# Kernel tuning notes

Hardware: AMD Instinct MI355X
Metric: run time of the kernel (lower is better)

## Reference

```python
import jax, jax.numpy as jnp
import numpy as np

NEG_SLOPE = 0.01  # torch F.leaky_relu default


def setup_inputs() -> dict:
    key = jax.random.key(0)
    k1, k2, k3, k4 = jax.random.split(key, 4)
    N, E, R, D = 100000, 1250000, 16, 64
    ego_embed = jax.random.normal(k1, (N, D), dtype=jnp.float32) * 0.1
    relation_weights = jax.random.normal(k2, (R, D, D), dtype=jnp.float32) * (1.0 / np.sqrt(D))
    edge_index = jax.random.randint(k3, (2, E), 0, N, dtype=jnp.int32)
    edge_type = jax.random.randint(k4, (E,), 0, R, dtype=jnp.int32)
    return {"ego_embed": ego_embed, "relation_weights": relation_weights,
            "edge_index": edge_index, "edge_type": edge_type}


def reference(ego_embed, relation_weights, edge_index, edge_type):
    head, tail = edge_index[0], edge_index[1]
    n_entities = ego_embed.shape[0]
    # Transform every node by every relation once ([R,N,D]) instead of
    # materializing the per-edge [E,D,D] weight gather the torch bmm implies;
    # same math: transformed_head[e] = ego_embed[head[e]] @ W[edge_type[e]].
    transformed_all = jnp.einsum('nd,rdk->rnk', ego_embed, relation_weights)
    transformed_head = transformed_all[edge_type, head]        # [E, D]
    tail_emb = ego_embed[tail]                                  # [E, D]
    scores = jax.nn.leaky_relu(jnp.sum(transformed_head * tail_emb, axis=1),
                               negative_slope=NEG_SLOPE)        # [E]
    exp_scores = jnp.exp(scores)                                # unnormalized attention
    denom = jax.ops.segment_sum(exp_scores, head, num_segments=n_entities)[head]
    norm_att = exp_scores / denom                               # segment softmax
    weighted = tail_emb * norm_att[:, None]                     # [E, D]
    # scatter_mean: segment sum / per-segment edge count (clamped to 1)
    summed = jax.ops.segment_sum(weighted, head, num_segments=n_entities)
    counts = jax.ops.segment_sum(jnp.ones_like(exp_scores), head, num_segments=n_entities)
    return summed / jnp.maximum(counts, 1.0)[:, None]
```

## Files before the change

kernel.cpp:

```cpp
#include <hip/hip_runtime.h>
#include <stdint.h>

#define NEG_SLOPE 0.01f
#define HPG 32
#define TSTR 72
#define BSH 8
#define NBMAX 512
#define K1CH 8192
#define CAP2 8192

typedef float f32x4 __attribute__((ext_vector_type(4)));
typedef short short8 __attribute__((ext_vector_type(8)));
typedef unsigned int u32;

#define DPPADD(v, ctrl) ((v) + __int_as_float(__builtin_amdgcn_update_dpp( \
        0, __float_as_int(v), (ctrl), 0xF, 0xF, true)))

__device__ inline short f2bf(float f) {
    union { float f; uint32_t u; } x; x.f = f;
    uint32_t r = x.u + 0x7FFF + ((x.u >> 16) & 1);
    return (short)(r >> 16);
}
__device__ inline float bf2f(unsigned short u) {
    union { uint32_t u; float f; } x; x.u = ((uint32_t)u) << 16; return x.f;
}

__global__ void __launch_bounds__(512) kA(
        const int* __restrict__ head, const int* __restrict__ tail,
        const int* __restrict__ etype, int E, int NB, int nblk,
        u32* __restrict__ staging, int* bucket_cur,
        const float* __restrict__ ego, unsigned short* __restrict__ ego_bf,
        int NE8, const float* __restrict__ rw, short* __restrict__ wfrag,
        int* __restrict__ head_off, int N) {
    int t = threadIdx.x;
    int bid = blockIdx.x;
    if (bid < nblk) {
        __shared__ int lcnt[NBMAX], lbase[NBMAX], lfill[NBMAX];
        for (int b = t; b < NBMAX; b += 512) lcnt[b] = 0;
        __syncthreads();
        long long base = (long long)bid * K1CH;
        #pragma unroll
        for (int s = 0; s < K1CH / 512; ++s) {
            long long e = base + t + s * 512;
            if (e < E) atomicAdd(&lcnt[head[e] >> BSH], 1);
        }
        __syncthreads();
        for (int b = t; b < NB; b += 512) {
            int c = lcnt[b];
            lbase[b] = c ? atomicAdd(&bucket_cur[b], c) : 0;
            lfill[b] = 0;
        }
        __syncthreads();
        #pragma unroll
        for (int s = 0; s < K1CH / 512; ++s) {
            long long e = base + t + s * 512;
            if (e < E) {
                int h = head[e];
                int bk = h >> BSH;
                int rk = atomicAdd(&lfill[bk], 1);
                int pos = lbase[bk] + rk;
                if (pos >= CAP2) pos = CAP2 - 1;
                staging[(size_t)bk * CAP2 + pos] =
                    (u32)tail[e] | ((u32)etype[e] << 20) | ((u32)(h & 255) << 24);
            }
        }
    } else {
        int ib = bid - nblk;
        if (ib == 0 && t == 0) head_off[N] = E;
        if (ib < 16) {
            int r = ib;
            int lane = t & 63;
            int c = lane & 15, q = lane >> 4;
            int pair = t >> 6;
            int t4 = pair >> 1, kh = pair & 1;
            int m = t4 * 16 + c;
            short8 f;
            for (int j = 0; j < 8; ++j) {
                int k = kh * 32 + q * 8 + j;
                f[j] = f2bf(rw[r * 4096 + k * 64 + m]);
            }
            *(short8*)(wfrag + ((size_t)((r * 4 + t4) * 2 + kh) * 64 + lane) * 8) = f;
        }
        int i = ib * 512 + t;
        if (i < NE8) {
            const float4* p = (const float4*)ego + (size_t)i * 2;
            float4 a = p[0], b = p[1];
            short8 v;
            v[0] = f2bf(a.x); v[1] = f2bf(a.y); v[2] = f2bf(a.z); v[3] = f2bf(a.w);
            v[4] = f2bf(b.x); v[5] = f2bf(b.y); v[6] = f2bf(b.z); v[7] = f2bf(b.w);
            *(short8*)(ego_bf + (size_t)i * 8) = v;
        }
    }
}

__global__ void __launch_bounds__(512) kB(
        const u32* __restrict__ staging, const int* __restrict__ bucket_cur,
        int* __restrict__ head_off, int* __restrict__ recs2, int N, int NB) {
    __shared__ int pre[NBMAX];
    __shared__ int lcnt[256], lofs[256], lfill[256];
    __shared__ u32 lrec[CAP2];
    int t = threadIdx.x;
    int b = blockIdx.x;
    if (t < 256) lcnt[t] = 0;
    int v = (t < NB) ? bucket_cur[t] : 0;
    pre[t] = v;
    __syncthreads();
    for (int off = 1; off < 512; off <<= 1) {
        int x = (t >= off) ? pre[t - off] : 0;
        __syncthreads();
        pre[t] += x;
        __syncthreads();
    }
    int cnt_raw = bucket_cur[b];
    int base_g = pre[b] - cnt_raw;
    int cntb = cnt_raw > CAP2 ? CAP2 : cnt_raw;
    int hbase = b << BSH;
    const u32* sb = staging + (size_t)b * CAP2;
    for (int t0 = t; t0 < cntb; t0 += 512) {
        u32 rec = sb[t0];
        lrec[t0] = rec;
        atomicAdd(&lcnt[rec >> 24], 1);
    }
    __syncthreads();
    if (t < 64) {
        int cl[4]; int cs = 0;
        #pragma unroll
        for (int j = 0; j < 4; ++j) { cl[j] = lcnt[t * 4 + j]; cs += cl[j]; }
        int inc = cs;
        for (int off = 1; off < 64; off <<= 1) {
            int u = __shfl_up(inc, off);
            if (t >= off) inc += u;
        }
        int run = inc - cs;
        #pragma unroll
        for (int j = 0; j < 4; ++j) {
            lofs[t * 4 + j] = run; lfill[t * 4 + j] = run; run += cl[j];
        }
    }
    __syncthreads();
    if (t < 256 && hbase + t < N)
        head_off[hbase + t] = base_g + lofs[t];
    for (int t0 = t; t0 < cntb; t0 += 512) {
        u32 rec = lrec[t0];
        int rk = atomicAdd(&lfill[rec >> 24], 1);
        recs2[base_g + rk] = (int)(rec & 0xFFFFFF);
    }
}

__global__ void __launch_bounds__(512, 4) k4_fused(
        const unsigned short* __restrict__ ego_bf,
        const short* __restrict__ wfrag,
        const int* __restrict__ recs2,
        const int* __restrict__ head_off,
        float* __restrict__ out, int N) {
    __shared__ unsigned short T[16 * HPG * TSTR];
    int tid = threadIdx.x;
    int wave = tid >> 6;
    int lane = tid & 63;
    int c = lane & 15, q = lane >> 4;
    int hb = blockIdx.x * HPG;

    for (int t = 0; t < 2; ++t) {
        int r = wave * 2 + t;
        const short* wp = wfrag + (size_t)r * 4096;
        short8 wf[4][2];
        #pragma unroll
        for (int t4 = 0; t4 < 4; ++t4)
            #pragma unroll
            for (int kh = 0; kh < 2; ++kh)
                wf[t4][kh] = *(const short8*)(wp + ((size_t)((t4 * 2 + kh) * 64 + lane)) * 8);
        #pragma unroll
        for (int hf = 0; hf < 2; ++hf) {
            int hrow = hb + hf * 16 + c;
            if (hrow >= N) hrow = N - 1;
            const unsigned short* hr = ego_bf + (size_t)hrow * 64;
            short8 b0 = *(const short8*)(hr + q * 8);
            short8 b1 = *(const short8*)(hr + 32 + q * 8);
            #pragma unroll
            for (int t4 = 0; t4 < 4; ++t4) {
                f32x4 a = {0.f, 0.f, 0.f, 0.f};
                a = __builtin_amdgcn_mfma_f32_16x16x32_bf16(wf[t4][0], b0, a, 0, 0, 0);
                a = __builtin_amdgcn_mfma_f32_16x16x32_bf16(wf[t4][1], b1, a, 0, 0, 0);
                ushort4 us;
                us.x = (unsigned short)f2bf(a[0]);
                us.y = (unsigned short)f2bf(a[1]);
                us.z = (unsigned short)f2bf(a[2]);
                us.w = (unsigned short)f2bf(a[3]);
                *(ushort4*)&T[(size_t)(r * HPG + hf * 16 + c) * TSTR + t4 * 16 + q * 4] = us;
            }
        }
    }
    __syncthreads();

    int hql = wave * 4 + q;
    int h = hb + hql;
    if (h >= N) return;
    int lq = c;
    int g2 = lq >> 3, c8 = lq & 7;
    int qb = q * 16;
    int s0 = head_off[h], s1 = head_off[h + 1];
    int cnt = s1 - s0;
    int nbt = (cnt + 15) >> 4;
    float acc[8] = {0.f, 0.f, 0.f, 0.f, 0.f, 0.f, 0.f, 0.f};
    float den = 0.f;

    auto loadRec = [&](int b) -> int {
        if (b >= nbt) return 0;
        int idx = s0 + b * 16 + lq;
        return (idx < s1) ? recs2[idx] : 0;
    };

    int rjA[8]; short8 rowsA[8];
    int recL1;
    {
        int recL0 = loadRec(0);
        #pragma unroll
        for (int j = 0; j < 8; ++j) rjA[j] = __shfl(recL0, qb + j * 2 + g2);
        #pragma unroll
        for (int j = 0; j < 8; ++j)
            rowsA[j] = *(const short8*)(ego_bf + (size_t)(rjA[j] & 0xFFFFF) * 64 + c8 * 8);
        recL1 = loadRec(1);
    }
    for (int b = 0; b < nbt; ++b) {
        int recL2 = loadRec(b + 2);
        int rjB[8]; short8 rowsB[8];
        #pragma unroll
        for (int j = 0; j < 8; ++j) rjB[j] = __shfl(recL1, qb + j * 2 + g2);
        #pragma unroll
        for (int j = 0; j < 8; ++j)
            rowsB[j] = *(const short8*)(ego_bf + (size_t)(rjB[j] & 0xFFFFF) * 64 + c8 * 8);
        int ng = s1 - (s0 + b * 16); if (ng > 16) ng = 16;
        #pragma unroll
        for (int sIt = 0; sIt < 8; ++sIt) {
            if (sIt * 2 < ng) {
                short8 trw = *(const short8*)&T[(size_t)(((u32)rjA[sIt] >> 20) * HPG + hql) * TSTR + c8 * 8];
                float rf[8];
                float sa = 0.f, sb = 0.f;
                #pragma unroll
                for (int k = 0; k < 4; ++k) {
                    rf[k] = bf2f((unsigned short)rowsA[sIt][k]);
                    sa += rf[k] * bf2f((unsigned short)trw[k]);
                }
                #pragma unroll
                for (int k = 4; k < 8; ++k) {
                    rf[k] = bf2f((unsigned short)rowsA[sIt][k]);
                    sb += rf[k] * bf2f((unsigned short)trw[k]);
                }
                float s = sa + sb;
                s = DPPADD(s, 0xB1);
                s = DPPADD(s, 0x4E);
                s = DPPADD(s, 0x141);
                float lr = s > 0.f ? s : NEG_SLOPE * s;
                float w = (sIt * 2 + g2 < ng) ? __expf(lr) : 0.f;
                den += w;
                #pragma unroll
                for (int k = 0; k < 8; ++k) acc[k] += w * rf[k];
            }
        }
        recL1 = recL2;
        #pragma unroll
        for (int j = 0; j < 8; ++j) { rjA[j] = rjB[j]; rowsA[j] = rowsB[j]; }
    }
    den = DPPADD(den, 0x128);
    #pragma unroll
    for (int k = 0; k < 8; ++k) acc[k] = DPPADD(acc[k], 0x128);
    if (g2 == 0) {
        float sc = (cnt > 0) ? 1.f / (den * (float)cnt) : 0.f;
        float4 v0 = {acc[0] * sc, acc[1] * sc, acc[2] * sc, acc[3] * sc};
        float4 v1 = {acc[4] * sc, acc[5] * sc, acc[6] * sc, acc[7] * sc};
        float* op = out + (size_t)h * 64 + c8 * 8;
        *(float4*)op = v0;
        *(float4*)(op + 4) = v1;
    }
}

extern "C" void kernel_launch(void* const* d_in, const int* in_sizes, int n_in,
                              void* d_out, int out_size, void* d_ws, size_t ws_size,
                              hipStream_t stream) {
    const float* ego = (const float*)d_in[0];
    const float* rw  = (const float*)d_in[1];
    const int* eidx  = (const int*)d_in[2];
    const int* etyp  = (const int*)d_in[3];
    int N = in_sizes[0] / 64;
    int E = in_sizes[3];
    const int* head = eidx;
    const int* tail = eidx + E;
    float* out = (float*)d_out;

    char* ws = (char*)d_ws;
    size_t o = 0;
    auto take = [&](size_t bytes) -> char* {
        char* p = ws + o;
        o = (o + bytes + 255) & ~(size_t)255;
        return p;
    };
    int NB = (N + (1 << BSH) - 1) >> BSH;
    if (NB > NBMAX) NB = NBMAX;
    int nblk = (E + K1CH - 1) / K1CH;
    int NE8 = N * 8;
    int nbI = (NE8 + 511) / 512;
    if (nbI < 16) nbI = 16;
    unsigned short* ego_bf = (unsigned short*)take((size_t)N * 64 * 2);
    short* wfrag    = (short*)take(16 * 4096 * 2);
    int* recs2      = (int*)take((size_t)E * 4);
    u32* staging    = (u32*)take((size_t)NB * CAP2 * 4);
    int* bucket_cur = (int*)take(NBMAX * 4);
    int* head_off   = (int*)take((size_t)(N + 1) * 4);
    (void)ws_size; (void)n_in; (void)out_size;

    hipMemsetAsync(bucket_cur, 0, NBMAX * 4, stream);
    kA<<<nblk + nbI, 512, 0, stream>>>(head, tail, etyp, E, NB, nblk,
                                       staging, bucket_cur,
                                       ego, ego_bf, NE8, rw, wfrag,
                                       head_off, N);
    kB<<<NB, 512, 0, stream>>>(staging, bucket_cur, head_off, recs2, N, NB);
    k4_fused<<<(N + HPG - 1) / HPG, 512, 0, stream>>>(ego_bf, wfrag, recs2,
                                                      head_off, out, N);
}
```

Baseline: 186.8 us.

## Fuse per-bucket sort into main kernel using 32-head buckets matching block tile

Shrinks the head buckets to 32 heads so each bucket lines up exactly with one k4_fused block. The second counting-sort kernel (kB) and the global recs2/head_off arrays go away. Each block now loads its bucket's staging records into LDS, builds per-head offsets with an LDS histogram and wave scan, and reads edge records from LDS instead of global memory. This removes a kernel launch and a full write and read of the edge array. The cost is 3200 buckets with 12KB+ LDS counters in kA, a per-bucket capacity cap of 1024 that would overflow on skewed heads, and more LDS use in the main kernel.

```diff
diff --git a/kernel.cpp b/kernel.cpp
--- a/kernel.cpp
+++ b/kernel.cpp
@@ -4,10 +4,10 @@
 #define NEG_SLOPE 0.01f
 #define HPG 32
 #define TSTR 72
-#define BSH 8
-#define NBMAX 512
-#define K1CH 8192
-#define CAP2 8192
+#define BSH 5
+#define NBMX 3200
+#define K1CH 16384
+#define CAP3 1024
 
 typedef float f32x4 __attribute__((ext_vector_type(4)));
 typedef short short8 __attribute__((ext_vector_type(8)));
@@ -30,13 +30,12 @@
         const int* __restrict__ etype, int E, int NB, int nblk,
         u32* __restrict__ staging, int* bucket_cur,
         const float* __restrict__ ego, unsigned short* __restrict__ ego_bf,
-        int NE8, const float* __restrict__ rw, short* __restrict__ wfrag,
-        int* __restrict__ head_off, int N) {
+        int NE8, const float* __restrict__ rw, short* __restrict__ wfrag) {
     int t = threadIdx.x;
     int bid = blockIdx.x;
     if (bid < nblk) {
-        __shared__ int lcnt[NBMAX], lbase[NBMAX], lfill[NBMAX];
-        for (int b = t; b < NBMAX; b += 512) lcnt[b] = 0;
+        __shared__ int lcnt[NBMX], lbase[NBMX], lfill[NBMX];
+        for (int b = t; b < NBMX; b += 512) lcnt[b] = 0;
         __syncthreads();
         long long base = (long long)bid * K1CH;
         #pragma unroll
@@ -59,14 +58,13 @@
                 int bk = h >> BSH;
                 int rk = atomicAdd(&lfill[bk], 1);
                 int pos = lbase[bk] + rk;
-                if (pos >= CAP2) pos = CAP2 - 1;
-                staging[(size_t)bk * CAP2 + pos] =
-                    (u32)tail[e] | ((u32)etype[e] << 20) | ((u32)(h & 255) << 24);
+                if (pos >= CAP3) pos = CAP3 - 1;
+                staging[(size_t)bk * CAP3 + pos] =
+                    (u32)tail[e] | ((u32)etype[e] << 20) | ((u32)(h & 31) << 24);
             }
         }
     } else {
         int ib = bid - nblk;
-        if (ib == 0 && t == 0) head_off[N] = E;
         if (ib < 16) {
             int r = ib;
             int lane = t & 63;
@@ -93,72 +91,43 @@
     }
 }
 
-__global__ void __launch_bounds__(512) kB(
-        const u32* __restrict__ staging, const int* __restrict__ bucket_cur,
-        int* __restrict__ head_off, int* __restrict__ recs2, int N, int NB) {
-    __shared__ int pre[NBMAX];
-    __shared__ int lcnt[256], lofs[256], lfill[256];
-    __shared__ u32 lrec[CAP2];
-    int t = threadIdx.x;
-    int b = blockIdx.x;
-    if (t < 256) lcnt[t] = 0;
-    int v = (t < NB) ? bucket_cur[t] : 0;
-    pre[t] = v;
-    __syncthreads();
-    for (int off = 1; off < 512; off <<= 1) {
-        int x = (t >= off) ? pre[t - off] : 0;
-        __syncthreads();
-        pre[t] += x;
-        __syncthreads();
-    }
-    int cnt_raw = bucket_cur[b];
-    int base_g = pre[b] - cnt_raw;
-    int cntb = cnt_raw > CAP2 ? CAP2 : cnt_raw;
-    int hbase = b << BSH;
-    const u32* sb = staging + (size_t)b * CAP2;
-    for (int t0 = t; t0 < cntb; t0 += 512) {
-        u32 rec = sb[t0];
-        lrec[t0] = rec;
-        atomicAdd(&lcnt[rec >> 24], 1);
-    }
-    __syncthreads();
-    if (t < 64) {
-        int cl[4]; int cs = 0;
-        #pragma unroll
-        for (int j = 0; j < 4; ++j) { cl[j] = lcnt[t * 4 + j]; cs += cl[j]; }
-        int inc = cs;
-        for (int off = 1; off < 64; off <<= 1) {
-            int u = __shfl_up(inc, off);
-            if (t >= off) inc += u;
-        }
-        int run = inc - cs;
-        #pragma unroll
-        for (int j = 0; j < 4; ++j) {
-            lofs[t * 4 + j] = run; lfill[t * 4 + j] = run; run += cl[j];
-        }
-    }
-    __syncthreads();
-    if (t < 256 && hbase + t < N)
-        head_off[hbase + t] = base_g + lofs[t];
-    for (int t0 = t; t0 < cntb; t0 += 512) {
-        u32 rec = lrec[t0];
-        int rk = atomicAdd(&lfill[rec >> 24], 1);
-        recs2[base_g + rk] = (int)(rec & 0xFFFFFF);
-    }
-}
-
 __global__ void __launch_bounds__(512, 4) k4_fused(
         const unsigned short* __restrict__ ego_bf,
         const short* __restrict__ wfrag,
-        const int* __restrict__ recs2,
-        const int* __restrict__ head_off,
+        const u32* __restrict__ staging,
+        const int* __restrict__ bucket_cur,
         float* __restrict__ out, int N) {
     __shared__ unsigned short T[16 * HPG * TSTR];
+    __shared__ u32 lrec[CAP3];
+    __shared__ int lhc[HPG], lofs[HPG], lcn[HPG];
     int tid = threadIdx.x;
     int wave = tid >> 6;
     int lane = tid & 63;
     int c = lane & 15, q = lane >> 4;
-    int hb = blockIdx.x * HPG;
+    int b = blockIdx.x;
+    int hb = b * HPG;
+
+    if (tid < HPG) lhc[tid] = 0;
+    __syncthreads();
+    int cnt_raw = bucket_cur[b];
+    int cntb = cnt_raw > CAP3 ? CAP3 : cnt_raw;
+    const u32* sb = staging + (size_t)b * CAP3;
+    u32 r0 = 0, r1 = 0; int rk0 = -1, rk1 = -1;
+    if (tid < cntb)       { r0 = sb[tid];       rk0 = atomicAdd(&lhc[r0 >> 24], 1); }
+    if (tid + 512 < cntb) { r1 = sb[tid + 512]; rk1 = atomicAdd(&lhc[r1 >> 24], 1); }
+    __syncthreads();
+    if (tid < 64) {
+        int v = (lane < HPG) ? lhc[lane] : 0;
+        int inc = v;
+        for (int off = 1; off < HPG; off <<= 1) {
+            int u = __shfl_up(inc, off);
+            if (lane >= off) inc += u;
+        }
+        if (lane < HPG) { lofs[lane] = inc - v; lcn[lane] = v; }
+    }
+    __syncthreads();
+    if (rk0 >= 0) lrec[lofs[r0 >> 24] + rk0] = r0;
+    if (rk1 >= 0) lrec[lofs[r1 >> 24] + rk1] = r1;
 
     for (int t = 0; t < 2; ++t) {
         int r = wave * 2 + t;
@@ -197,45 +166,41 @@
     if (h >= N) return;
     int lq = c;
     int g2 = lq >> 3, c8 = lq & 7;
-    int qb = q * 16;
-    int s0 = head_off[h], s1 = head_off[h + 1];
-    int cnt = s1 - s0;
+    int s0 = lofs[hql];
+    int cnt = lcn[hql];
     int nbt = (cnt + 15) >> 4;
     float acc[8] = {0.f, 0.f, 0.f, 0.f, 0.f, 0.f, 0.f, 0.f};
     float den = 0.f;
 
-    auto loadRec = [&](int b) -> int {
-        if (b >= nbt) return 0;
-        int idx = s0 + b * 16 + lq;
-        return (idx < s1) ? recs2[idx] : 0;
+    auto recAt = [&](int b2, int j) -> u32 {
+        int idx = b2 * 16 + j * 2 + g2;
+        return (idx < cnt) ? lrec[s0 + idx] : 0;
     };
 
-    int rjA[8]; short8 rowsA[8];
-    int recL1;
-    {
-        int recL0 = loadRec(0);
-        #pragma unroll
-        for (int j = 0; j < 8; ++j) rjA[j] = __shfl(recL0, qb + j * 2 + g2);
-        #pragma unroll
-        for (int j = 0; j < 8; ++j)
-            rowsA[j] = *(const short8*)(ego_bf + (size_t)(rjA[j] & 0xFFFFF) * 64 + c8 * 8);
-        recL1 = loadRec(1);
-    }
-    for (int b = 0; b < nbt; ++b) {
-        int recL2 = loadRec(b + 2);
-        int rjB[8]; short8 rowsB[8];
-        #pragma unroll
-        for (int j = 0; j < 8; ++j) rjB[j] = __shfl(recL1, qb + j * 2 + g2);
-        #pragma unroll
-        for (int j = 0; j < 8; ++j)
-            rowsB[j] = *(const short8*)(ego_bf + (size_t)(rjB[j] & 0xFFFFF) * 64 + c8 * 8);
-        int ng = s1 - (s0 + b * 16); if (ng > 16) ng = 16;
+    u32 rjA[8]; short8 rowsA[8];
+    #pragma unroll
+    for (int j = 0; j < 8; ++j) rjA[j] = recAt(0, j);
+    #pragma unroll
+    for (int j = 0; j < 8; ++j)
+        rowsA[j] = *(const short8*)(ego_bf + (size_t)(rjA[j] & 0xFFFFF) * 64 + c8 * 8);
+    for (int b2 = 0; b2 < nbt; ++b2) {
+        u32 rjB[8]; short8 rowsB[8];
+        bool more = (b2 + 1 < nbt);
+        if (more) {
+            #pragma unroll
+            for (int j = 0; j < 8; ++j) rjB[j] = recAt(b2 + 1, j);
+            #pragma unroll
+            for (int j = 0; j < 8; ++j)
+                rowsB[j] = *(const short8*)(ego_bf + (size_t)(rjB[j] & 0xFFFFF) * 64 + c8 * 8);
+        }
+        int ng = cnt - b2 * 16; if (ng > 16) ng = 16;
         #pragma unroll
         for (int sIt = 0; sIt < 8; ++sIt) {
             if (sIt * 2 < ng) {
-                short8 trw = *(const short8*)&T[(size_t)(((u32)rjA[sIt] >> 20) * HPG + hql) * TSTR + c8 * 8];
+                int ty = (rjA[sIt] >> 20) & 15;
+                short8 trw = *(const short8*)&T[(size_t)(ty * HPG + hql) * TSTR + c8 * 8];
                 float rf[8];
-                float sa = 0.f, sb = 0.f;
+                float sa = 0.f, sb2 = 0.f;
                 #pragma unroll
                 for (int k = 0; k < 4; ++k) {
                     rf[k] = bf2f((unsigned short)rowsA[sIt][k]);
@@ -244,9 +209,9 @@
                 #pragma unroll
                 for (int k = 4; k < 8; ++k) {
                     rf[k] = bf2f((unsigned short)rowsA[sIt][k]);
-                    sb += rf[k] * bf2f((unsigned short)trw[k]);
+                    sb2 += rf[k] * bf2f((unsigned short)trw[k]);
                 }
-                float s = sa + sb;
+                float s = sa + sb2;
                 s = DPPADD(s, 0xB1);
                 s = DPPADD(s, 0x4E);
                 s = DPPADD(s, 0x141);
@@ -257,9 +222,10 @@
                 for (int k = 0; k < 8; ++k) acc[k] += w * rf[k];
             }
         }
-        recL1 = recL2;
-        #pragma unroll
-        for (int j = 0; j < 8; ++j) { rjA[j] = rjB[j]; rowsA[j] = rowsB[j]; }
+        if (more) {
+            #pragma unroll
+            for (int j = 0; j < 8; ++j) { rjA[j] = rjB[j]; rowsA[j] = rowsB[j]; }
+        }
     }
     den = DPPADD(den, 0x128);
     #pragma unroll
@@ -294,26 +260,22 @@
         o = (o + bytes + 255) & ~(size_t)255;
         return p;
     };
-    int NB = (N + (1 << BSH) - 1) >> BSH;
-    if (NB > NBMAX) NB = NBMAX;
+    int NB = (N + HPG - 1) >> BSH;
+    if (NB > NBMX) NB = NBMX;
     int nblk = (E + K1CH - 1) / K1CH;
     int NE8 = N * 8;
     int nbI = (NE8 + 511) / 512;
     if (nbI < 16) nbI = 16;
     unsigned short* ego_bf = (unsigned short*)take((size_t)N * 64 * 2);
     short* wfrag    = (short*)take(16 * 4096 * 2);
-    int* recs2      = (int*)take((size_t)E * 4);
-    u32* staging    = (u32*)take((size_t)NB * CAP2 * 4);
-    int* bucket_cur = (int*)take(NBMAX * 4);
-    int* head_off   = (int*)take((size_t)(N + 1) * 4);
+    u32* staging    = (u32*)take((size_t)NB * CAP3 * 4);
+    int* bucket_cur = (int*)take((size_t)NBMX * 4);
     (void)ws_size; (void)n_in; (void)out_size;
 
-    hipMemsetAsync(bucket_cur, 0, NBMAX * 4, stream);
+    hipMemsetAsync(bucket_cur, 0, (size_t)NBMX * 4, stream);
     kA<<<nblk + nbI, 512, 0, stream>>>(head, tail, etyp, E, NB, nblk,
                                        staging, bucket_cur,
-                                       ego, ego_bf, NE8, rw, wfrag,
-                                       head_off, N);
-    kB<<<NB, 512, 0, stream>>>(staging, bucket_cur, head_off, recs2, N, NB);
-    k4_fused<<<(N + HPG - 1) / HPG, 512, 0, stream>>>(ego_bf, wfrag, recs2,
-                                                      head_off, out, N);
-}
+                                       ego, ego_bf, NE8, rw, wfrag);
+    k4_fused<<<NB, 512, 0, stream>>>(ego_bf, wfrag, staging, bucket_cur,
+                                     out, N);
+}
```

New measurement: 196.6 us. 5.2% more time.

## Split each head's edges across two wave halves with 1024-thread blocks and XOR-swizzled LDS

Applied to the files above, without the earlier changes.

The fused attention kernel now runs 1024 threads per block. Each wave computes one relation's transform tile, and the edge list of every head is split in half between two groups of waves. The partial sums and denominators are combined through shared memory before the output is written. The padded transform table is replaced by an XOR-swizzled layout to avoid bank conflicts without the padding. This halves the serial edge loop per head and adds an extra barrier plus a shared-memory reduction. It also raises register pressure, since launch_bounds(1024,8) must fit in a tighter per-thread budget.

```diff
diff --git a/kernel.cpp b/kernel.cpp
--- a/kernel.cpp
+++ b/kernel.cpp
@@ -3,7 +3,6 @@
 
 #define NEG_SLOPE 0.01f
 #define HPG 32
-#define TSTR 72
 #define BSH 8
 #define NBMAX 512
 #define K1CH 8192
@@ -147,21 +146,22 @@
     }
 }
 
-__global__ void __launch_bounds__(512, 4) k4_fused(
+__global__ void __launch_bounds__(1024, 8) k4_fused(
         const unsigned short* __restrict__ ego_bf,
         const short* __restrict__ wfrag,
         const int* __restrict__ recs2,
         const int* __restrict__ head_off,
         float* __restrict__ out, int N) {
-    __shared__ unsigned short T[16 * HPG * TSTR];
+    __shared__ unsigned short T[16 * HPG * 64];
+    __shared__ float cmb[HPG][8][9];
     int tid = threadIdx.x;
     int wave = tid >> 6;
     int lane = tid & 63;
     int c = lane & 15, q = lane >> 4;
     int hb = blockIdx.x * HPG;
 
-    for (int t = 0; t < 2; ++t) {
-        int r = wave * 2 + t;
+    {
+        int r = wave;
         const short* wp = wfrag + (size_t)r * 4096;
         short8 wf[4][2];
         #pragma unroll
@@ -176,6 +176,7 @@
             const unsigned short* hr = ego_bf + (size_t)hrow * 64;
             short8 b0 = *(const short8*)(hr + q * 8);
             short8 b1 = *(const short8*)(hr + 32 + q * 8);
+            int row = r * HPG + hf * 16 + c;
             #pragma unroll
             for (int t4 = 0; t4 < 4; ++t4) {
                 f32x4 a = {0.f, 0.f, 0.f, 0.f};
@@ -186,28 +187,34 @@
                 us.y = (unsigned short)f2bf(a[1]);
                 us.z = (unsigned short)f2bf(a[2]);
                 us.w = (unsigned short)f2bf(a[3]);
-                *(ushort4*)&T[(size_t)(r * HPG + hf * 16 + c) * TSTR + t4 * 16 + q * 4] = us;
+                int chunk = t4 * 2 + (q >> 1);
+                int ha = row * 64 + ((chunk ^ (row & 7)) * 8) + (q & 1) * 4;
+                *(ushort4*)&T[ha] = us;
             }
         }
     }
     __syncthreads();
 
-    int hql = wave * 4 + q;
+    int hql = (wave & 7) * 4 + q;
+    int halfsel = wave >> 3;
     int h = hb + hql;
-    if (h >= N) return;
+    bool act = (h < N);
     int lq = c;
     int g2 = lq >> 3, c8 = lq & 7;
     int qb = q * 16;
-    int s0 = head_off[h], s1 = head_off[h + 1];
-    int cnt = s1 - s0;
+    int s0g = 0, cntF = 0;
+    if (act) { s0g = head_off[h]; cntF = head_off[h + 1] - s0g; }
+    int m = cntF >> 1;
+    int a0 = s0g + (halfsel ? m : 0);
+    int cnt = halfsel ? (cntF - m) : m;
     int nbt = (cnt + 15) >> 4;
     float acc[8] = {0.f, 0.f, 0.f, 0.f, 0.f, 0.f, 0.f, 0.f};
     float den = 0.f;
 
     auto loadRec = [&](int b) -> int {
         if (b >= nbt) return 0;
-        int idx = s0 + b * 16 + lq;
-        return (idx < s1) ? recs2[idx] : 0;
+        int idx = b * 16 + lq;
+        return (idx < cnt) ? recs2[a0 + idx] : 0;
     };
 
     int rjA[8]; short8 rowsA[8];
@@ -229,13 +236,15 @@
         #pragma unroll
         for (int j = 0; j < 8; ++j)
             rowsB[j] = *(const short8*)(ego_bf + (size_t)(rjB[j] & 0xFFFFF) * 64 + c8 * 8);
-        int ng = s1 - (s0 + b * 16); if (ng > 16) ng = 16;
+        int ng = cnt - b * 16; if (ng > 16) ng = 16;
         #pragma unroll
         for (int sIt = 0; sIt < 8; ++sIt) {
             if (sIt * 2 < ng) {
-                short8 trw = *(const short8*)&T[(size_t)(((u32)rjA[sIt] >> 20) * HPG + hql) * TSTR + c8 * 8];
+                int row2 = ((rjA[sIt] >> 20) & 15) * HPG + hql;
+                int ha = row2 * 64 + ((c8 ^ (row2 & 7)) * 8);
+                short8 trw = *(const short8*)&T[ha];
                 float rf[8];
-                float sa = 0.f, sb = 0.f;
+                float sa = 0.f, sb2 = 0.f;
                 #pragma unroll
                 for (int k = 0; k < 4; ++k) {
                     rf[k] = bf2f((unsigned short)rowsA[sIt][k]);
@@ -244,9 +253,9 @@
                 #pragma unroll
                 for (int k = 4; k < 8; ++k) {
                     rf[k] = bf2f((unsigned short)rowsA[sIt][k]);
-                    sb += rf[k] * bf2f((unsigned short)trw[k]);
+                    sb2 += rf[k] * bf2f((unsigned short)trw[k]);
                 }
-                float s = sa + sb;
+                float s = sa + sb2;
                 s = DPPADD(s, 0xB1);
                 s = DPPADD(s, 0x4E);
                 s = DPPADD(s, 0x141);
@@ -264,8 +273,18 @@
     den = DPPADD(den, 0x128);
     #pragma unroll
     for (int k = 0; k < 8; ++k) acc[k] = DPPADD(acc[k], 0x128);
-    if (g2 == 0) {
-        float sc = (cnt > 0) ? 1.f / (den * (float)cnt) : 0.f;
+
+    if (halfsel && g2 == 0) {
+        #pragma unroll
+        for (int k = 0; k < 8; ++k) cmb[hql][c8][k] = acc[k];
+        cmb[hql][c8][8] = den;
+    }
+    __syncthreads();
+    if (!halfsel && g2 == 0 && act) {
+        #pragma unroll
+        for (int k = 0; k < 8; ++k) acc[k] += cmb[hql][c8][k];
+        den += cmb[hql][c8][8];
+        float sc = (cntF > 0) ? 1.f / (den * (float)cntF) : 0.f;
         float4 v0 = {acc[0] * sc, acc[1] * sc, acc[2] * sc, acc[3] * sc};
         float4 v1 = {acc[4] * sc, acc[5] * sc, acc[6] * sc, acc[7] * sc};
         float* op = out + (size_t)h * 64 + c8 * 8;
@@ -314,6 +333,6 @@
                                        ego, ego_bf, NE8, rw, wfrag,
                                        head_off, N);
     kB<<<NB, 512, 0, stream>>>(staging, bucket_cur, head_off, recs2, N, NB);
-    k4_fused<<<(N + HPG - 1) / HPG, 512, 0, stream>>>(ego_bf, wfrag, recs2,
-                                                      head_off, out, N);
-}
+    k4_fused<<<(N + HPG - 1) / HPG, 1024, 0, stream>>>(ego_bf, wfrag, recs2,
+                                                       head_off, out, N);
+}
```

After: 405.9 us. +117.3%, slower.
